# Performance work log

Hardware: AMD Instinct MI355X
Metric: run time of the kernel (lower is better)

## Reference

```python
import jax, jax.numpy as jnp
import numpy as np

B, S, D, H = 2, 2048, 1024, 16
DH = D // H
CAUSAL = True


def setup_inputs() -> dict:
    key = jax.random.key(0)
    ks = jax.random.split(key, 11)
    s = 1.0 / np.sqrt(D)
    return {
        "x": jax.random.normal(ks[0], (B, S, D), dtype=jnp.float32),
        "Wq": jax.random.uniform(ks[1], (D, D), jnp.float32, -s, s),
        "bq": jax.random.uniform(ks[2], (D,), jnp.float32, -s, s),
        "Wk": jax.random.uniform(ks[3], (D, D), jnp.float32, -s, s),
        "bk": jax.random.uniform(ks[4], (D,), jnp.float32, -s, s),
        "Wv": jax.random.uniform(ks[5], (D, D), jnp.float32, -s, s),
        "bv": jax.random.uniform(ks[6], (D,), jnp.float32, -s, s),
        "Wo": jax.random.uniform(ks[7], (D, D), jnp.float32, -s, s),
        "bo": jax.random.uniform(ks[8], (D,), jnp.float32, -s, s),
        "ln_g": jnp.ones((D,), jnp.float32),
        "ln_b": jnp.zeros((D,), jnp.float32),
    }


def reference(x, Wq, bq, Wk, bk, Wv, bv, Wo, bo, ln_g, ln_b):
    scale = np.sqrt(DH).astype(np.float32)
    # projections -> [B, H, S, DH]
    def proj(W, b):
        return (x @ W.T + b).reshape(B, S, H, DH).transpose(0, 2, 1, 3)
    Q, K, V = proj(Wq, bq), proj(Wk, bk), proj(Wv, bv)
    scores = jnp.einsum("bhsd,bhtd->bhst", Q, K) / scale  # [B,H,S,S]
    if CAUSAL:
        causal = jnp.tril(jnp.ones((S, S), dtype=bool))
        scores = jnp.where(causal, scores, -jnp.inf)
    attn = jax.nn.softmax(scores, axis=-1)
    ctx = jnp.einsum("bhst,bhtd->bhsd", attn, V)
    ctx = ctx.transpose(0, 2, 1, 3).reshape(B, S, D)
    attn_out = ctx @ Wo.T + bo
    y = x + attn_out
    mu = jnp.mean(y, axis=-1, keepdims=True)
    var = jnp.mean(jnp.square(y - mu), axis=-1, keepdims=True)
    return (y - mu) / jnp.sqrt(var + 1e-5) * ln_g + ln_b
```

## Files before the change

### kernel.cpp

```cpp
#include <hip/hip_runtime.h>
#include <stdint.h>

#define B_   2
#define S_   2048
#define D_   1024
#define H_   16
#define DH_  64
#define MTOK (B_*S_)

typedef __attribute__((ext_vector_type(8))) short  short8v;
typedef __attribute__((ext_vector_type(4))) float  f32x4;
typedef __attribute__((ext_vector_type(16))) float f32x16;
typedef __attribute__((ext_vector_type(4))) unsigned int uint4v;

__device__ __forceinline__ unsigned short f2bf(float f) {
  unsigned int u = __builtin_bit_cast(unsigned int, f);
  unsigned int r = (u + 0x7fffu + ((u >> 16) & 1u)) >> 16;
  return (unsigned short)r;
}

__device__ __forceinline__ f32x4 zero4() { f32x4 v = {0.f, 0.f, 0.f, 0.f}; return v; }
__device__ __forceinline__ f32x16 zero16() {
  f32x16 v;
#pragma unroll
  for (int i = 0; i < 16; ++i) v[i] = 0.f;
  return v;
}

__device__ __forceinline__ unsigned int cvtpk(float lo, float hi) {
  unsigned int d;
  asm("v_cvt_pk_bf16_f32 %0, %1, %2" : "=v"(d) : "v"(lo), "v"(hi));
  return d;
}
__device__ __forceinline__ void plswap(unsigned int& a, unsigned int& b) {
  asm("v_permlane32_swap_b32 %0, %1" : "+v"(a), "+v"(b));
}

__device__ __forceinline__ void gload16(const void* g, void* l) {
  __builtin_amdgcn_global_load_lds(
      (const __attribute__((address_space(1))) void*)g,
      (__attribute__((address_space(3))) void*)l, 16, 0, 0);
}

__global__ void cvt_all_kernel(
    const float* __restrict__ x,
    const float* __restrict__ w0, const float* __restrict__ w1,
    const float* __restrict__ w2, const float* __restrict__ w3,
    unsigned short* __restrict__ xb,
    unsigned short* __restrict__ o0, unsigned short* __restrict__ o1,
    unsigned short* __restrict__ o2, unsigned short* __restrict__ o3)
{
  const int total = MTOK * D_ / 4 + D_ * D_;
  for (int i = blockIdx.x * blockDim.x + threadIdx.x; i < total;
       i += gridDim.x * blockDim.x) {
    const float* in;
    unsigned short* out;
    int off;
    if (i < MTOK * D_ / 4) {
      in = x; out = xb; off = i;
    } else {
      int j = i - MTOK * D_ / 4;
      int w = j >> 18;
      off = j & 262143;
      in  = (w == 0) ? w0 : (w == 1) ? w1 : (w == 2) ? w2 : w3;
      out = (w == 0) ? o0 : (w == 1) ? o1 : (w == 2) ? o2 : o3;
    }
    float4 v = reinterpret_cast<const float4*>(in)[off];
    ushort4 o;
    o.x = f2bf(v.x); o.y = f2bf(v.y); o.z = f2bf(v.z); o.w = f2bf(v.w);
    reinterpret_cast<ushort4*>(out)[off] = o;
  }
}

__device__ __forceinline__ void stage_gemm32(
    const unsigned short* __restrict__ A, const unsigned short* __restrict__ Bt,
    int K, int m0, int n0, int k0, unsigned short* As, unsigned short* Bs, int tid)
{
#pragma unroll
  for (int it = 0; it < 2; ++it) {
    int fa = it * 256 + tid;
    int row = fa >> 2, slot = fa & 3;
    int gs = slot ^ ((row >> 1) & 3);
    gload16(A + (size_t)(m0 + row) * K + k0 + gs * 8, (char*)As + fa * 16);
  }
#pragma unroll
  for (int it = 0; it < 2; ++it) {
    int fa = it * 256 + tid;
    int row = fa >> 2, slot = fa & 3;
    int gs = slot ^ ((row >> 1) & 3);
    gload16(Bt + (size_t)(n0 + row) * K + k0 + gs * 8, (char*)Bs + fa * 16);
  }
}

__device__ __forceinline__ void gemm_mainloop(
    const unsigned short* __restrict__ A, const unsigned short* __restrict__ Bt,
    int K, int m0, int n0, unsigned short* As, unsigned short* Bs, f32x4 acc[4][4])
{
  const int tid = threadIdx.x;
  const int lane = tid & 63, wid = tid >> 6;
  const int wr = wid >> 1, wc = wid & 1;
  const int l15 = lane & 15, g = lane >> 4;

#pragma unroll
  for (int mi = 0; mi < 4; ++mi)
#pragma unroll
    for (int ni = 0; ni < 4; ++ni) acc[mi][ni] = zero4();

  const int nk = K >> 5;
  stage_gemm32(A, Bt, K, m0, n0, 0, As, Bs, tid);
  asm volatile("s_waitcnt vmcnt(0)" ::: "memory");
  __builtin_amdgcn_s_barrier();
  asm volatile("" ::: "memory");

  for (int k = 0; k < nk; ++k) {
    if (k + 1 < nk)
      stage_gemm32(A, Bt, K, m0, n0, (k + 1) << 5,
                   As + ((k + 1) & 1) * 4096, Bs + ((k + 1) & 1) * 4096, tid);
    const char* Ab = (const char*)(As + (k & 1) * 4096);
    const char* Bb = (const char*)(Bs + (k & 1) * 4096);
    short8v af[4], bfr[4];
#pragma unroll
    for (int mi = 0; mi < 4; ++mi) {
      int row = wr * 64 + mi * 16 + l15;
      int slot = g ^ ((row >> 1) & 3);
      af[mi] = *(const short8v*)(Ab + row * 64 + slot * 16);
    }
#pragma unroll
    for (int ni = 0; ni < 4; ++ni) {
      int row = wc * 64 + ni * 16 + l15;
      int slot = g ^ ((row >> 1) & 3);
      bfr[ni] = *(const short8v*)(Bb + row * 64 + slot * 16);
    }
#pragma unroll
    for (int mi = 0; mi < 4; ++mi)
#pragma unroll
      for (int ni = 0; ni < 4; ++ni)
        acc[mi][ni] = __builtin_amdgcn_mfma_f32_16x16x32_bf16(af[mi], bfr[ni], acc[mi][ni], 0, 0, 0);
    asm volatile("s_waitcnt vmcnt(0)" ::: "memory");
    __builtin_amdgcn_s_barrier();
    asm volatile("" ::: "memory");
  }
}

__global__ __launch_bounds__(256) void gemm_qkv_kernel(
    const unsigned short* __restrict__ xb,
    const unsigned short* __restrict__ wqb, const unsigned short* __restrict__ wkb,
    const unsigned short* __restrict__ wvb,
    const float* __restrict__ bq, const float* __restrict__ bk, const float* __restrict__ bv,
    unsigned short* __restrict__ Qb, unsigned short* __restrict__ Kb, unsigned short* __restrict__ VTb)
{
  __shared__ __align__(16) unsigned short As[2 * 128 * 32];
  __shared__ __align__(16) unsigned short Bs[2 * 128 * 32];
  const int flat = blockIdx.x;
  const int xcd = flat & 7, off = flat >> 3;
  const int mtile = xcd * 4 + (off / 24);
  const int ntile = off % 24;
  const int z = ntile >> 3;
  const int m0 = mtile * 128, n0 = (ntile & 7) * 128;
  const unsigned short* Bt = (z == 0) ? wqb : (z == 1) ? wkb : wvb;
  const float* bias = (z == 0) ? bq : (z == 1) ? bk : bv;
  const float scl = (z == 0) ? 0.180336880f : 1.0f;

  f32x4 acc[4][4];
  gemm_mainloop(xb, Bt, D_, m0, n0, As, Bs, acc);

  const int tid = threadIdx.x, lane = tid & 63, wid = tid >> 6;
  const int wr = wid >> 1, wc = wid & 1, l15 = lane & 15, g = lane >> 4;
#pragma unroll
  for (int ni = 0; ni < 4; ++ni) {
    int n = n0 + wc * 64 + ni * 16 + l15;
    float bia = bias[n];
    int hh = n >> 6, dh = n & 63;
#pragma unroll
    for (int mi = 0; mi < 4; ++mi) {
      int mbase = m0 + wr * 64 + mi * 16 + 4 * g;
      int b = mbase >> 11;
      int s0 = mbase & 2047;
      if (z < 2) {
        unsigned short* o = (z == 0) ? Qb : Kb;
#pragma unroll
        for (int r = 0; r < 4; ++r) {
          float v = (acc[mi][ni][r] + bia) * scl;
          o[(((size_t)(b * H_ + hh) * S_ + (s0 + r)) << 6) + dh] = f2bf(v);
        }
      } else {
        ushort4 o;
        o.x = f2bf(acc[mi][ni][0] + bia);
        o.y = f2bf(acc[mi][ni][1] + bia);
        o.z = f2bf(acc[mi][ni][2] + bia);
        o.w = f2bf(acc[mi][ni][3] + bia);
        *(ushort4*)(VTb + ((size_t)(b * H_ + hh) * DH_ + dh) * S_ + s0) = o;
      }
    }
  }
}

__device__ __forceinline__ void stage_tile128_w8(
    const unsigned short* Kh, const unsigned short* Vh, int t0, char* base, int tid)
{
#pragma unroll
  for (int it = 0; it < 2; ++it) {
    int fa = it * 512 + tid;
    int row = fa >> 3, slot = fa & 7, gs = slot ^ (row & 7);
    gload16(Kh + (size_t)(t0 + row) * DH_ + gs * 8, base + fa * 16);
  }
#pragma unroll
  for (int it = 0; it < 2; ++it) {
    int fa = it * 512 + tid;
    int row = fa >> 4, slot = fa & 15;
    int gs = slot ^ (row & 7);
    gload16(Vh + (size_t)row * S_ + t0 + gs * 8, base + 16384 + fa * 16);
  }
}

__global__ __launch_bounds__(512, 4) void attn_kernel(
    const unsigned short* __restrict__ Qb, const unsigned short* __restrict__ Kb,
    const unsigned short* __restrict__ VTb, unsigned short* __restrict__ ctxb)
{
  __shared__ __align__(16) char smem[65536];
  const int tid = threadIdx.x, lane = tid & 63, wid = tid >> 6;
  const int qw = wid & 3, kp = wid >> 2;
  const int l31 = lane & 31, h = lane >> 5;
  const int fid = blockIdx.x;
  const int bh = (fid & 7) * 4 + ((fid >> 3) & 3);
  const int qpos = fid >> 5;
  const int qi = (qpos < 8) ? qpos : 23 - qpos;
  const int qblk = qi * 128;
  const int q0w = qblk + qw * 32;
  const int qg = q0w + l31;
  const unsigned short* Qh = Qb + (size_t)bh * S_ * DH_;
  const unsigned short* Kh = Kb + (size_t)bh * S_ * DH_;
  const unsigned short* Vh = VTb + (size_t)bh * DH_ * S_;

  short8v qf[4];
#pragma unroll
  for (int kk = 0; kk < 4; ++kk)
    qf[kk] = *(const short8v*)(Qh + (size_t)qg * DH_ + kk * 16 + h * 8);

  f32x16 ctx0 = zero16(), ctx1 = zero16();
  float mrun = -3e38f, lrun = 0.f;

  const int nt = qi + 1;

  stage_tile128_w8(Kh, Vh, 0, smem, tid);
  asm volatile("s_waitcnt vmcnt(0)" ::: "memory");
  __builtin_amdgcn_s_barrier();
  asm volatile("" ::: "memory");

  for (int t = 0; t < nt; ++t) {
    if (t + 1 < nt) stage_tile128_w8(Kh, Vh, (t + 1) << 7, smem + (((t + 1) & 1) * 32768), tid);
    const char* Kbuf = smem + (t & 1) * 32768;
    const char* Vbuf = Kbuf + 16384;
    const int t0 = (t << 7) + (kp << 6);
    if (t0 <= q0w + 31) {
      const char* Kt = Kbuf + kp * 8192;

      f32x16 s0 = zero16(), s1 = zero16();
      __builtin_amdgcn_s_setprio(1);
#pragma unroll
      for (int kk = 0; kk < 4; ++kk) {
        int slot = (2 * kk + h) ^ (l31 & 7);
        short8v kf0 = *(const short8v*)(Kt + l31 * 128 + slot * 16);
        short8v kf1 = *(const short8v*)(Kt + (32 + l31) * 128 + slot * 16);
        s0 = __builtin_amdgcn_mfma_f32_32x32x16_bf16(kf0, qf[kk], s0, 0, 0, 0);
        s1 = __builtin_amdgcn_mfma_f32_32x32x16_bf16(kf1, qf[kk], s1, 0, 0, 0);
      }
      __builtin_amdgcn_s_setprio(0);
      if (t0 + 63 > q0w) {
#pragma unroll
        for (int r = 0; r < 16; ++r) {
          int k0i = (r & 3) + 8 * (r >> 2) + 4 * h;
          if (t0 + k0i > qg) s0[r] = -1e30f;
          if (t0 + k0i + 32 > qg) s1[r] = -1e30f;
        }
      }
      float tm;
      {
        float m01[8];
#pragma unroll
        for (int r = 0; r < 8; ++r)
          m01[r] = fmaxf(fmaxf(s0[r], s0[r + 8]), fmaxf(s1[r], s1[r + 8]));
        float a = fmaxf(fmaxf(m01[0], m01[1]), fmaxf(m01[2], m01[3]));
        float b = fmaxf(fmaxf(m01[4], m01[5]), fmaxf(m01[6], m01[7]));
        tm = fmaxf(a, b);
      }
      tm = fmaxf(tm, __shfl_xor(tm, 32));

      if (!__all(tm <= mrun + 8.f)) {
        float mnew = fmaxf(mrun, tm);
        float al = exp2f(mrun - mnew);
#pragma unroll
        for (int r = 0; r < 16; ++r) { ctx0[r] *= al; ctx1[r] *= al; }
        lrun *= al;
        mrun = mnew;
      }
      float p[32];
      float psa0 = 0.f, psa1 = 0.f, psa2 = 0.f, psa3 = 0.f;
#pragma unroll
      for (int r = 0; r < 16; r += 4) {
        p[r + 0] = exp2f(s0[r + 0] - mrun); psa0 += p[r + 0];
        p[r + 1] = exp2f(s0[r + 1] - mrun); psa1 += p[r + 1];
        p[r + 2] = exp2f(s0[r + 2] - mrun); psa2 += p[r + 2];
        p[r + 3] = exp2f(s0[r + 3] - mrun); psa3 += p[r + 3];
      }
#pragma unroll
      for (int r = 0; r < 16; r += 4) {
        p[16 + r + 0] = exp2f(s1[r + 0] - mrun); psa0 += p[16 + r + 0];
        p[16 + r + 1] = exp2f(s1[r + 1] - mrun); psa1 += p[16 + r + 1];
        p[16 + r + 2] = exp2f(s1[r + 2] - mrun); psa2 += p[16 + r + 2];
        p[16 + r + 3] = exp2f(s1[r + 3] - mrun); psa3 += p[16 + r + 3];
      }
      float ps = (psa0 + psa1) + (psa2 + psa3);
      ps += __shfl_xor(ps, 32);
      lrun += ps;

      unsigned int pk[16];
#pragma unroll
      for (int m = 0; m < 16; ++m) pk[m] = cvtpk(p[2 * m], p[2 * m + 1]);
#pragma unroll
      for (int base = 0; base < 16; base += 4) {
        plswap(pk[base + 0], pk[base + 2]);
        plswap(pk[base + 1], pk[base + 3]);
      }
      __builtin_amdgcn_s_setprio(1);
#pragma unroll
      for (int dt = 0; dt < 2; ++dt) {
        int row = dt * 32 + l31;
#pragma unroll
        for (int kt = 0; kt < 4; ++kt) {
          int slot = (2 * kt + h) ^ (row & 7);
          short8v vf = *(const short8v*)(Vbuf + row * 256 + kp * 128 + slot * 16);
          uint4v u = {pk[4 * kt], pk[4 * kt + 1], pk[4 * kt + 2], pk[4 * kt + 3]};
          short8v pf = __builtin_bit_cast(short8v, u);
          if (dt == 0) ctx0 = __builtin_amdgcn_mfma_f32_32x32x16_bf16(vf, pf, ctx0, 0, 0, 0);
          else         ctx1 = __builtin_amdgcn_mfma_f32_32x32x16_bf16(vf, pf, ctx1, 0, 0, 0);
        }
      }
      __builtin_amdgcn_s_setprio(0);
    }
    asm volatile("s_waitcnt vmcnt(0)" ::: "memory");
    __builtin_amdgcn_s_barrier();
    asm volatile("" ::: "memory");
  }

  float* cws = (float*)smem + qw * 2176;
  if (kp == 1) {
#pragma unroll
    for (int r = 0; r < 16; ++r) {
      cws[r * 64 + lane]        = ctx0[r];
      cws[(16 + r) * 64 + lane] = ctx1[r];
    }
    cws[32 * 64 + lane] = mrun;
    cws[33 * 64 + lane] = lrun;
  }
  __syncthreads();
  if (kp == 0) {
    float pm = cws[32 * 64 + lane], pl = cws[33 * 64 + lane];
    float m  = fmaxf(mrun, pm);
    float sa = exp2f(mrun - m), sb = exp2f(pm - m);
    float L  = lrun * sa + pl * sb;
    float cf[32];
#pragma unroll
    for (int r = 0; r < 16; ++r) {
      cf[r]      = ctx0[r] * sa + cws[r * 64 + lane] * sb;
      cf[16 + r] = ctx1[r] * sa + cws[(16 + r) * 64 + lane] * sb;
    }
    const int b = bh >> 4, hcol = (bh & 15) * 64;
    unsigned short* orow = ctxb + (((size_t)(b * S_ + qg)) << 10) + hcol;
    float invL = 1.0f / L;
#pragma unroll
    for (int j = 0; j < 8; ++j) {
      uint2 w;
      w.x = cvtpk(cf[4 * j + 0] * invL, cf[4 * j + 1] * invL);
      w.y = cvtpk(cf[4 * j + 2] * invL, cf[4 * j + 3] * invL);
      *(uint2*)(orow + 32 * (j >> 2) + 8 * (j & 3) + 4 * h) = w;
    }
  }
}

__global__ __launch_bounds__(256) void gemm_out_kernel(
    const unsigned short* __restrict__ ctxb, const unsigned short* __restrict__ wob,
    const float* __restrict__ bo, const float* __restrict__ x, float* __restrict__ y)
{
  __shared__ __align__(16) unsigned short As[2 * 128 * 32];
  __shared__ __align__(16) unsigned short Bs[2 * 128 * 32];
  const int flat = blockIdx.x;
  const int xcd = flat & 7, off = flat >> 3;
  const int m0 = (xcd * 4 + (off >> 3)) * 128;
  const int n0 = (off & 7) * 128;
  f32x4 acc[4][4];
  gemm_mainloop(ctxb, wob, D_, m0, n0, As, Bs, acc);

  const int tid = threadIdx.x, lane = tid & 63, wid = tid >> 6;
  const int wr = wid >> 1, wc = wid & 1, l15 = lane & 15, g = lane >> 4;
#pragma unroll
  for (int ni = 0; ni < 4; ++ni) {
    int n = n0 + wc * 64 + ni * 16 + l15;
    float bia = bo[n];
#pragma unroll
    for (int mi = 0; mi < 4; ++mi) {
      int mbase = m0 + wr * 64 + mi * 16 + 4 * g;
#pragma unroll
      for (int r = 0; r < 4; ++r) {
        size_t idx = ((size_t)(mbase + r) << 10) + n;
        y[idx] = acc[mi][ni][r] + bia + x[idx];
      }
    }
  }
}

__global__ __launch_bounds__(256) void ln_kernel(
    float* __restrict__ y, const float* __restrict__ gw, const float* __restrict__ bw)
{
  const int lane = threadIdx.x & 63, w = threadIdx.x >> 6;
  const int row = blockIdx.x * 4 + w;
  float* p = y + ((size_t)row << 10);
  float4 v[4];
  float s = 0.f, s2 = 0.f;
#pragma unroll
  for (int i = 0; i < 4; ++i) {
    v[i] = *(const float4*)(p + i * 256 + lane * 4);
    s  += (v[i].x + v[i].y) + (v[i].z + v[i].w);
    s2 += (v[i].x * v[i].x + v[i].y * v[i].y) + (v[i].z * v[i].z + v[i].w * v[i].w);
  }
#pragma unroll
  for (int d = 1; d < 64; d <<= 1) { s += __shfl_xor(s, d); s2 += __shfl_xor(s2, d); }
  float mu  = s * (1.f / 1024.f);
  float var = s2 * (1.f / 1024.f) - mu * mu;
  float rstd = rsqrtf(var + 1e-5f);
#pragma unroll
  for (int i = 0; i < 4; ++i) {
    float4 gv = *(const float4*)(gw + i * 256 + lane * 4);
    float4 bv = *(const float4*)(bw + i * 256 + lane * 4);
    float4 o;
    o.x = (v[i].x - mu) * rstd * gv.x + bv.x;
    o.y = (v[i].y - mu) * rstd * gv.y + bv.y;
    o.z = (v[i].z - mu) * rstd * gv.z + bv.z;
    o.w = (v[i].w - mu) * rstd * gv.w + bv.w;
    *(float4*)(p + i * 256 + lane * 4) = o;
  }
}

extern "C" void kernel_launch(void* const* d_in, const int* in_sizes, int n_in,
                              void* d_out, int out_size, void* d_ws, size_t ws_size,
                              hipStream_t stream) {
  const float* x   = (const float*)d_in[0];
  const float* Wq  = (const float*)d_in[1];
  const float* bq  = (const float*)d_in[2];
  const float* Wk  = (const float*)d_in[3];
  const float* bk  = (const float*)d_in[4];
  const float* Wv  = (const float*)d_in[5];
  const float* bv  = (const float*)d_in[6];
  const float* Wo  = (const float*)d_in[7];
  const float* bo  = (const float*)d_in[8];
  const float* lng = (const float*)d_in[9];
  const float* lnb = (const float*)d_in[10];
  float* out = (float*)d_out;

  char* ws = (char*)d_ws;
  unsigned short* xb  = (unsigned short*)ws;                 ws += (size_t)MTOK * D_ * 2;
  unsigned short* wqb = (unsigned short*)ws;                 ws += (size_t)D_ * D_ * 2;
  unsigned short* wkb = (unsigned short*)ws;                 ws += (size_t)D_ * D_ * 2;
  unsigned short* wvb = (unsigned short*)ws;                 ws += (size_t)D_ * D_ * 2;
  unsigned short* wob = (unsigned short*)ws;                 ws += (size_t)D_ * D_ * 2;
  unsigned short* Qb  = (unsigned short*)ws;                 ws += (size_t)B_ * H_ * S_ * DH_ * 2;
  unsigned short* Kb  = (unsigned short*)ws;                 ws += (size_t)B_ * H_ * S_ * DH_ * 2;
  unsigned short* VTb = (unsigned short*)ws;                 ws += (size_t)B_ * H_ * DH_ * S_ * 2;
  unsigned short* ctxb = (unsigned short*)ws;                ws += (size_t)MTOK * D_ * 2;

  cvt_all_kernel<<<2048, 256, 0, stream>>>(
      x, Wq, Wk, Wv, Wo, xb, wqb, wkb, wvb, wob);

  gemm_qkv_kernel<<<dim3(768), 256, 0, stream>>>(
      xb, wqb, wkb, wvb, bq, bk, bv, Qb, Kb, VTb);

  attn_kernel<<<dim3((S_ / 128) * B_ * H_), 512, 0, stream>>>(Qb, Kb, VTb, ctxb);

  gemm_out_kernel<<<dim3(256), 256, 0, stream>>>(ctxb, wob, bo, x, out);

  ln_kernel<<<MTOK / 4, 256, 0, stream>>>(out, lng, lnb);
}
```

Baseline: 122.1 us.

## Split attention keys across four wave groups with 1024-thread blocks

The attention kernel doubles its block size to 16 waves. Each wave now handles a 32-key slice of the 128-key tile instead of a 64-key slice, so each wave does half the QK and PV MFMAs per tile and each thread stages one K and one V chunk per tile. The goal is more waves in flight to hide latency and to shorten each wave's serial softmax work. In exchange, the end of the kernel needs a two-stage shared-memory merge of the four partial softmax states, with extra barriers and a larger LDS footprint, which may limit how many blocks fit on a CU.

Result: slower. 378.4 us (+210.0%).

```diff
diff --git a/kernel.cpp b/kernel.cpp
--- a/kernel.cpp
+++ b/kernel.cpp
@@ -195,29 +195,27 @@
   }
 }
 
-__device__ __forceinline__ void stage_tile128_w8(
+__device__ __forceinline__ void stage_tile128_w16(
     const unsigned short* Kh, const unsigned short* Vh, int t0, char* base, int tid)
 {
-#pragma unroll
-  for (int it = 0; it < 2; ++it) {
-    int fa = it * 512 + tid;
+  {
+    int fa = tid;
     int row = fa >> 3, slot = fa & 7, gs = slot ^ (row & 7);
     gload16(Kh + (size_t)(t0 + row) * DH_ + gs * 8, base + fa * 16);
   }
-#pragma unroll
-  for (int it = 0; it < 2; ++it) {
-    int fa = it * 512 + tid;
+  {
+    int fa = tid;
     int row = fa >> 4, slot = fa & 15;
     int gs = slot ^ (row & 7);
     gload16(Vh + (size_t)row * S_ + t0 + gs * 8, base + 16384 + fa * 16);
   }
 }
 
-__global__ __launch_bounds__(512, 4) void attn_kernel(
+__global__ __launch_bounds__(1024, 8) void attn_kernel(
     const unsigned short* __restrict__ Qb, const unsigned short* __restrict__ Kb,
     const unsigned short* __restrict__ VTb, unsigned short* __restrict__ ctxb)
 {
-  __shared__ __align__(16) char smem[65536];
+  __shared__ __align__(16) char smem[73728];
   const int tid = threadIdx.x, lane = tid & 63, wid = tid >> 6;
   const int qw = wid & 3, kp = wid >> 2;
   const int l31 = lane & 31, h = lane >> 5;
@@ -242,47 +240,42 @@
 
   const int nt = qi + 1;
 
-  stage_tile128_w8(Kh, Vh, 0, smem, tid);
+  stage_tile128_w16(Kh, Vh, 0, smem, tid);
   asm volatile("s_waitcnt vmcnt(0)" ::: "memory");
   __builtin_amdgcn_s_barrier();
   asm volatile("" ::: "memory");
 
   for (int t = 0; t < nt; ++t) {
-    if (t + 1 < nt) stage_tile128_w8(Kh, Vh, (t + 1) << 7, smem + (((t + 1) & 1) * 32768), tid);
+    if (t + 1 < nt) stage_tile128_w16(Kh, Vh, (t + 1) << 7, smem + (((t + 1) & 1) * 32768), tid);
     const char* Kbuf = smem + (t & 1) * 32768;
     const char* Vbuf = Kbuf + 16384;
-    const int t0 = (t << 7) + (kp << 6);
+    const int t0 = (t << 7) + (kp << 5);
     if (t0 <= q0w + 31) {
-      const char* Kt = Kbuf + kp * 8192;
-
-      f32x16 s0 = zero16(), s1 = zero16();
+      const int krow = kp * 32 + l31;
+
+      f32x16 s0 = zero16();
       __builtin_amdgcn_s_setprio(1);
 #pragma unroll
       for (int kk = 0; kk < 4; ++kk) {
-        int slot = (2 * kk + h) ^ (l31 & 7);
-        short8v kf0 = *(const short8v*)(Kt + l31 * 128 + slot * 16);
-        short8v kf1 = *(const short8v*)(Kt + (32 + l31) * 128 + slot * 16);
+        int slot = (2 * kk + h) ^ (krow & 7);
+        short8v kf0 = *(const short8v*)(Kbuf + krow * 128 + slot * 16);
         s0 = __builtin_amdgcn_mfma_f32_32x32x16_bf16(kf0, qf[kk], s0, 0, 0, 0);
-        s1 = __builtin_amdgcn_mfma_f32_32x32x16_bf16(kf1, qf[kk], s1, 0, 0, 0);
       }
       __builtin_amdgcn_s_setprio(0);
-      if (t0 + 63 > q0w) {
+      if (t0 + 31 > q0w) {
 #pragma unroll
         for (int r = 0; r < 16; ++r) {
           int k0i = (r & 3) + 8 * (r >> 2) + 4 * h;
           if (t0 + k0i > qg) s0[r] = -1e30f;
-          if (t0 + k0i + 32 > qg) s1[r] = -1e30f;
         }
       }
       float tm;
       {
-        float m01[8];
-#pragma unroll
-        for (int r = 0; r < 8; ++r)
-          m01[r] = fmaxf(fmaxf(s0[r], s0[r + 8]), fmaxf(s1[r], s1[r + 8]));
-        float a = fmaxf(fmaxf(m01[0], m01[1]), fmaxf(m01[2], m01[3]));
-        float b = fmaxf(fmaxf(m01[4], m01[5]), fmaxf(m01[6], m01[7]));
-        tm = fmaxf(a, b);
+        float m01[4];
+#pragma unroll
+        for (int r = 0; r < 4; ++r)
+          m01[r] = fmaxf(fmaxf(s0[r], s0[r + 4]), fmaxf(s0[r + 8], s0[r + 12]));
+        tm = fmaxf(fmaxf(m01[0], m01[1]), fmaxf(m01[2], m01[3]));
       }
       tm = fmaxf(tm, __shfl_xor(tm, 32));
 
@@ -294,7 +287,7 @@
         lrun *= al;
         mrun = mnew;
       }
-      float p[32];
+      float p[16];
       float psa0 = 0.f, psa1 = 0.f, psa2 = 0.f, psa3 = 0.f;
 #pragma unroll
       for (int r = 0; r < 16; r += 4) {
@@ -303,22 +296,15 @@
         p[r + 2] = exp2f(s0[r + 2] - mrun); psa2 += p[r + 2];
         p[r + 3] = exp2f(s0[r + 3] - mrun); psa3 += p[r + 3];
       }
-#pragma unroll
-      for (int r = 0; r < 16; r += 4) {
-        p[16 + r + 0] = exp2f(s1[r + 0] - mrun); psa0 += p[16 + r + 0];
-        p[16 + r + 1] = exp2f(s1[r + 1] - mrun); psa1 += p[16 + r + 1];
-        p[16 + r + 2] = exp2f(s1[r + 2] - mrun); psa2 += p[16 + r + 2];
-        p[16 + r + 3] = exp2f(s1[r + 3] - mrun); psa3 += p[16 + r + 3];
-      }
       float ps = (psa0 + psa1) + (psa2 + psa3);
       ps += __shfl_xor(ps, 32);
       lrun += ps;
 
-      unsigned int pk[16];
-#pragma unroll
-      for (int m = 0; m < 16; ++m) pk[m] = cvtpk(p[2 * m], p[2 * m + 1]);
-#pragma unroll
-      for (int base = 0; base < 16; base += 4) {
+      unsigned int pk[8];
+#pragma unroll
+      for (int m = 0; m < 8; ++m) pk[m] = cvtpk(p[2 * m], p[2 * m + 1]);
+#pragma unroll
+      for (int base = 0; base < 8; base += 4) {
         plswap(pk[base + 0], pk[base + 2]);
         plswap(pk[base + 1], pk[base + 3]);
       }
@@ -327,9 +313,9 @@
       for (int dt = 0; dt < 2; ++dt) {
         int row = dt * 32 + l31;
 #pragma unroll
-        for (int kt = 0; kt < 4; ++kt) {
-          int slot = (2 * kt + h) ^ (row & 7);
-          short8v vf = *(const short8v*)(Vbuf + row * 256 + kp * 128 + slot * 16);
+        for (int kt = 0; kt < 2; ++kt) {
+          int gslot = (kp * 4 + 2 * kt + h) ^ (row & 7);
+          short8v vf = *(const short8v*)(Vbuf + row * 256 + gslot * 16);
           uint4v u = {pk[4 * kt], pk[4 * kt + 1], pk[4 * kt + 2], pk[4 * kt + 3]};
           short8v pf = __builtin_bit_cast(short8v, u);
           if (dt == 0) ctx0 = __builtin_amdgcn_mfma_f32_32x32x16_bf16(vf, pf, ctx0, 0, 0, 0);
@@ -343,37 +329,66 @@
     asm volatile("" ::: "memory");
   }
 
-  float* cws = (float*)smem + qw * 2176;
-  if (kp == 1) {
-#pragma unroll
-    for (int r = 0; r < 16; ++r) {
-      cws[r * 64 + lane]        = ctx0[r];
-      cws[(16 + r) * 64 + lane] = ctx1[r];
-    }
-    cws[32 * 64 + lane] = mrun;
-    cws[33 * 64 + lane] = lrun;
+  float* base = (float*)smem;
+  {
+    float* cw = base + ((qw << 1) | (kp >> 1)) * 2176;
+    if (kp & 1) {
+#pragma unroll
+      for (int r = 0; r < 16; ++r) {
+        cw[r * 64 + lane]        = ctx0[r];
+        cw[(16 + r) * 64 + lane] = ctx1[r];
+      }
+      cw[32 * 64 + lane] = mrun;
+      cw[33 * 64 + lane] = lrun;
+    }
+    __syncthreads();
+    if (!(kp & 1)) {
+      float pm = cw[32 * 64 + lane], pl = cw[33 * 64 + lane];
+      float m  = fmaxf(mrun, pm);
+      float sa = exp2f(mrun - m), sb = exp2f(pm - m);
+      lrun = lrun * sa + pl * sb;
+#pragma unroll
+      for (int r = 0; r < 16; ++r) {
+        ctx0[r] = ctx0[r] * sa + cw[r * 64 + lane] * sb;
+        ctx1[r] = ctx1[r] * sa + cw[(16 + r) * 64 + lane] * sb;
+      }
+      mrun = m;
+    }
   }
   __syncthreads();
-  if (kp == 0) {
-    float pm = cws[32 * 64 + lane], pl = cws[33 * 64 + lane];
-    float m  = fmaxf(mrun, pm);
-    float sa = exp2f(mrun - m), sb = exp2f(pm - m);
-    float L  = lrun * sa + pl * sb;
-    float cf[32];
-#pragma unroll
-    for (int r = 0; r < 16; ++r) {
-      cf[r]      = ctx0[r] * sa + cws[r * 64 + lane] * sb;
-      cf[16 + r] = ctx1[r] * sa + cws[(16 + r) * 64 + lane] * sb;
-    }
-    const int b = bh >> 4, hcol = (bh & 15) * 64;
-    unsigned short* orow = ctxb + (((size_t)(b * S_ + qg)) << 10) + hcol;
-    float invL = 1.0f / L;
-#pragma unroll
-    for (int j = 0; j < 8; ++j) {
-      uint2 w;
-      w.x = cvtpk(cf[4 * j + 0] * invL, cf[4 * j + 1] * invL);
-      w.y = cvtpk(cf[4 * j + 2] * invL, cf[4 * j + 3] * invL);
-      *(uint2*)(orow + 32 * (j >> 2) + 8 * (j & 3) + 4 * h) = w;
+  {
+    float* cw2 = base + (((qw << 1) | 1)) * 2176;
+    if (kp == 2) {
+#pragma unroll
+      for (int r = 0; r < 16; ++r) {
+        cw2[r * 64 + lane]        = ctx0[r];
+        cw2[(16 + r) * 64 + lane] = ctx1[r];
+      }
+      cw2[32 * 64 + lane] = mrun;
+      cw2[33 * 64 + lane] = lrun;
+    }
+    __syncthreads();
+    if (kp == 0) {
+      float pm = cw2[32 * 64 + lane], pl = cw2[33 * 64 + lane];
+      float m  = fmaxf(mrun, pm);
+      float sa = exp2f(mrun - m), sb = exp2f(pm - m);
+      float L  = lrun * sa + pl * sb;
+      float cf[32];
+#pragma unroll
+      for (int r = 0; r < 16; ++r) {
+        cf[r]      = ctx0[r] * sa + cw2[r * 64 + lane] * sb;
+        cf[16 + r] = ctx1[r] * sa + cw2[(16 + r) * 64 + lane] * sb;
+      }
+      const int b = bh >> 4, hcol = (bh & 15) * 64;
+      unsigned short* orow = ctxb + (((size_t)(b * S_ + qg)) << 10) + hcol;
+      float invL = 1.0f / L;
+#pragma unroll
+      for (int j = 0; j < 8; ++j) {
+        uint2 w;
+        w.x = cvtpk(cf[4 * j + 0] * invL, cf[4 * j + 1] * invL);
+        w.y = cvtpk(cf[4 * j + 2] * invL, cf[4 * j + 3] * invL);
+        *(uint2*)(orow + 32 * (j >> 2) + 8 * (j & 3) + 4 * h) = w;
+      }
     }
   }
 }
@@ -474,7 +489,7 @@
   gemm_qkv_kernel<<<dim3(768), 256, 0, stream>>>(
       xb, wqb, wkb, wvb, bq, bk, bv, Qb, Kb, VTb);
 
-  attn_kernel<<<dim3((S_ / 128) * B_ * H_), 512, 0, stream>>>(Qb, Kb, VTb, ctxb);
+  attn_kernel<<<dim3((S_ / 128) * B_ * H_), 1024, 0, stream>>>(Qb, Kb, VTb, ctxb);
 
   gemm_out_kernel<<<dim3(256), 256, 0, stream>>>(ctxb, wob, bo, x, out);
 
```
